# Optimization experiments

Measured on AMD Instinct MI355X. Metric: run time of the kernel, lower is better.

## Reference

```python
import jax, jax.numpy as jnp
import numpy as np

DIM = 1024
NUM_HEADS = 16
HEAD_DIM = DIM // NUM_HEADS


def setup_inputs() -> dict:
    key = jax.random.key(0)
    k1, k2, k3, k4, k5 = jax.random.split(key, 5)
    B, N, C = 4, 4096, DIM
    s = 1.0 / np.sqrt(C)
    return {
        "x": jax.random.normal(k1, (B, N, C), dtype=jnp.float32),
        "W_qkv": jax.random.uniform(k2, (C, 3 * C), dtype=jnp.float32, minval=-s, maxval=s),
        "b_qkv": jax.random.uniform(k3, (3 * C,), dtype=jnp.float32, minval=-s, maxval=s),
        "W_proj": jax.random.uniform(k4, (C, C), dtype=jnp.float32, minval=-s, maxval=s),
        "b_proj": jax.random.uniform(k5, (C,), dtype=jnp.float32, minval=-s, maxval=s),
    }


def reference(x, W_qkv, b_qkv, W_proj, b_proj):
    B, N, C = x.shape
    H, D = NUM_HEADS, HEAD_DIM
    qkv = x @ W_qkv + b_qkv                      # [B,N,3C]
    qkv = qkv.reshape(B, N, 3, H, D).transpose(2, 0, 3, 1, 4)  # [3,B,H,N,D]
    q, k, v = qkv[0], qkv[1], qkv[2]
    q = jax.nn.softmax(q, axis=-1)               # softmax over head_dim
    k = jax.nn.softmax(k, axis=-2)               # softmax over sequence N
    context = jnp.einsum('bhnd,bhne->bhde', k, v)  # [B,H,D,D]
    out = jnp.einsum('bhnd,bhde->bhne', q, context)  # [B,H,N,D]
    out = out.transpose(0, 2, 1, 3).reshape(B, N, C)
    return out @ W_proj + b_proj
```

## Files before the change

### kernel.cpp

```cpp
#include <hip/hip_runtime.h>

#define BBATCH 4
#define SEQ 4096
#define CC 1024
#define HH 16
#define DD 64
#define TOKENS 16384
#define QKV3 3072

typedef __attribute__((ext_vector_type(8))) short short8;
typedef __attribute__((ext_vector_type(4))) float floatx4;

__device__ __forceinline__ unsigned short f2bf(float x) {
    unsigned int u = __float_as_uint(x);
    u += 0x7fff + ((u >> 16) & 1);
    return (unsigned short)(u >> 16);
}
__device__ __forceinline__ float bf2f(unsigned short h) {
    return __uint_as_float((unsigned int)h << 16);
}

__device__ __forceinline__ void gload_lds16(const void* g, void* l) {
    __builtin_amdgcn_global_load_lds(
        (const __attribute__((address_space(1))) unsigned int*)g,
        (__attribute__((address_space(3))) unsigned int*)l, 16, 0, 0);
}

__global__ __launch_bounds__(256) void cvt_bf16_kernel(
    const float* __restrict__ X, unsigned short* __restrict__ Y, long n4)
{
    long i = (long)blockIdx.x * 256 + threadIdx.x;
    if (i >= n4) return;
    float4 v = *reinterpret_cast<const float4*>(&X[i * 4]);
    ushort4 h;
    h.x = f2bf(v.x); h.y = f2bf(v.y); h.z = f2bf(v.z); h.w = f2bf(v.w);
    *reinterpret_cast<ushort4*>(&Y[i * 4]) = h;
}

__global__ __launch_bounds__(256) void transpose_bf16_kernel(
    const float* __restrict__ W, int K, int N, unsigned short* __restrict__ T)
{
    __shared__ unsigned short Lh[32][36];
    const int k0 = blockIdx.y * 32, n0 = blockIdx.x * 32;
    const int t = threadIdx.x;
    const int r = t >> 3, c4 = (t & 7) * 4;

    float4 w = *reinterpret_cast<const float4*>(&W[(size_t)(k0 + r) * N + n0 + c4]);
    Lh[r][c4 + 0] = f2bf(w.x);
    Lh[r][c4 + 1] = f2bf(w.y);
    Lh[r][c4 + 2] = f2bf(w.z);
    Lh[r][c4 + 3] = f2bf(w.w);
    __syncthreads();

    const int rn = t >> 3, ck = (t & 7) * 4;
    ushort4 h4;
    h4.x = Lh[ck + 0][rn]; h4.y = Lh[ck + 1][rn];
    h4.z = Lh[ck + 2][rn]; h4.w = Lh[ck + 3][rn];
    *reinterpret_cast<ushort4*>(&T[(size_t)(n0 + rn) * K + k0 + ck]) = h4;
}

__global__ __launch_bounds__(512) void gemm_qkv_kernel(
    const unsigned short* __restrict__ A, int lda,
    const unsigned short* __restrict__ Bt, int ldb,
    const float* __restrict__ bias,
    unsigned short* __restrict__ Qo, unsigned short* __restrict__ Ko,
    unsigned short* __restrict__ Vo)
{
    __shared__ unsigned short smem[65536];

    const int t = threadIdx.x;
    const int wave = t >> 6, lane = t & 63;

    const int gx = gridDim.x;
    const int nwg = gx * gridDim.y;
    const int id0 = blockIdx.y * gx + blockIdx.x;
    const int cpx = nwg >> 3;
    const int swzid = (id0 & 7) * cpx + (id0 >> 3);
    const int bx = swzid % gx, by = swzid / gx;

    const int row0 = by * 256, col0 = bx * 256;
    const int wave_m = wave >> 2, wave_n = wave & 3;

    const unsigned short* Bp = Bt;

    const int fr  = lane & 15;
    const int fqb = (lane >> 4) << 4;
    const int sm  = (fr & 7) << 4;
    const int ck0 = ((0  + fqb) ^ sm) >> 1;
    const int ck1 = ((64 + fqb) ^ sm) >> 1;
    const int aRow = (wave_m * 128 + fr) * 64;
    const int bRow = (wave_n * 64 + fr) * 64;

    int srow[2], scol[2];
#pragma unroll
    for (int e = 0; e < 2; e++) {
        const int P  = (wave << 10) + (lane << 4) + (e << 13);
        const int r  = P >> 7;
        const int pc = P & 127;
        srow[e] = r;
        scol[e] = (pc ^ ((r & 7) << 4)) >> 1;
    }

    auto STAGE_PART = [&](int kt, int buf, int part) {
        const int isB = part >> 1, half = part & 1;
        const unsigned short* p = isB ? Bp : A;
        const int r0 = isB ? col0 : row0;
        const int ld = isB ? ldb : lda;
        const int ldsOff = buf * 32768 + isB * 16384 + half * 8192 + wave * 512;
#pragma unroll
        for (int e = 0; e < 2; e++)
            gload_lds16(&p[(size_t)(r0 + half * 128 + srow[e]) * ld
                           + ((kt & 15) << 6) + scol[e]],
                        &smem[ldsOff + e * 4096]);
    };

    floatx4 acc[8][4];
#pragma unroll
    for (int i = 0; i < 8; i++)
#pragma unroll
        for (int j = 0; j < 4; j++) acc[i][j] = (floatx4)0.0f;

    short8 a[4][2], bl[2][2], bh[2][2];

#define RDA(BUF, IH)                                                          \
    _Pragma("unroll") for (int ii = 0; ii < 4; ii++) {                        \
        a[ii][0] = *reinterpret_cast<const short8*>(                          \
            &smem[(BUF) * 32768 + aRow + ((IH) * 64 + ii * 16) * 64 + ck0]);  \
        a[ii][1] = *reinterpret_cast<const short8*>(                          \
            &smem[(BUF) * 32768 + aRow + ((IH) * 64 + ii * 16) * 64 + ck1]);  \
    }
#define RDB(BUF, JH, DST)                                                     \
    _Pragma("unroll") for (int jj = 0; jj < 2; jj++) {                        \
        DST[jj][0] = *reinterpret_cast<const short8*>(                        \
            &smem[(BUF) * 32768 + 16384 + bRow + ((JH) * 32 + jj * 16) * 64 + ck0]); \
        DST[jj][1] = *reinterpret_cast<const short8*>(                        \
            &smem[(BUF) * 32768 + 16384 + bRow + ((JH) * 32 + jj * 16) * 64 + ck1]); \
    }
#define MFMA_Q(IH, JH, BB)                                                    \
    __builtin_amdgcn_s_setprio(1);                                            \
    _Pragma("unroll") for (int ii = 0; ii < 4; ii++)                          \
    _Pragma("unroll") for (int jj = 0; jj < 2; jj++) {                        \
        acc[(IH)*4+ii][(JH)*2+jj] = __builtin_amdgcn_mfma_f32_16x16x32_bf16(  \
            a[ii][0], BB[jj][0], acc[(IH)*4+ii][(JH)*2+jj], 0, 0, 0);         \
        acc[(IH)*4+ii][(JH)*2+jj] = __builtin_amdgcn_mfma_f32_16x16x32_bf16(  \
            a[ii][1], BB[jj][1], acc[(IH)*4+ii][(JH)*2+jj], 0, 0, 0);         \
    }                                                                         \
    __builtin_amdgcn_s_setprio(0);
#define BARRIER __builtin_amdgcn_s_barrier()
#define WAIT_LGKM asm volatile("s_waitcnt lgkmcnt(0)" ::: "memory")
#define WAIT_VM2  asm volatile("s_waitcnt vmcnt(2)" ::: "memory")

#define KTILE(CUR, OTH, TN, TX)                                               \
    {                                                                         \
        RDA(CUR, 0); RDB(CUR, 0, bl);                                         \
        STAGE_PART(TN, OTH, 1);                                               \
        BARRIER; WAIT_LGKM; MFMA_Q(0, 0, bl); BARRIER;                        \
        RDB(CUR, 1, bh);                                                      \
        STAGE_PART(TN, OTH, 2);                                               \
        BARRIER; WAIT_LGKM; MFMA_Q(0, 1, bh); BARRIER;                        \
        RDA(CUR, 1);                                                          \
        STAGE_PART(TN, OTH, 3);                                               \
        BARRIER; WAIT_LGKM; MFMA_Q(1, 1, bh); BARRIER;                        \
        STAGE_PART(TX, CUR, 0);                                               \
        WAIT_VM2;                                                             \
        BARRIER;                                                              \
        MFMA_Q(1, 0, bl);                                                     \
        BARRIER;                                                              \
    }

    STAGE_PART(0, 0, 0); STAGE_PART(0, 0, 1);
    STAGE_PART(0, 0, 2); STAGE_PART(0, 0, 3);
    STAGE_PART(1, 1, 0);
    WAIT_VM2;
    BARRIER;

#pragma unroll 1
    for (int it = 0; it < 8; it++) {
        const int t1 = 2 * it + 1, t2 = 2 * it + 2, t3 = 2 * it + 3;
        KTILE(0, 1, t1, t2);
        KTILE(1, 0, t2, t3);
    }

#undef KTILE
#undef WAIT_VM2
#undef WAIT_LGKM
#undef BARRIER
#undef MFMA_Q
#undef RDB
#undef RDA

    const int cn = lane & 15, cq = (lane >> 4) * 4;

    __syncthreads();

#pragma unroll
    for (int j = 0; j < 4; j++) {
        const int colL = wave_n * 64 + j * 16 + cn;
        const float bv = bias[col0 + colL];
#pragma unroll
        for (int i = 0; i < 8; i++)
#pragma unroll
            for (int r = 0; r < 4; r++) {
                const int lr = wave_m * 128 + i * 16 + cq + r;
                smem[lr * 256 + (colL ^ ((lr & 7) << 3))] = f2bf(acc[i][j][r] + bv);
            }
    }
    __syncthreads();

    {
        unsigned short* outp = (bx < 4) ? Qo : ((bx < 8) ? Ko : Vo);
        const bool isQ = (bx < 4);
        const int R = t >> 1, half = t & 1;
        const size_t obase = (size_t)(row0 + R) * CC + (col0 & 1023) + half * 128;
        unsigned short* orow = &outp[obase];

#pragma unroll
        for (int g = 0; g < 2; g++) {
            short8 bufv[8];
            const int cbase = half * 16 + g * 8;
#pragma unroll
            for (int k = 0; k < 8; k++)
                bufv[k] = *reinterpret_cast<const short8*>(
                    &smem[R * 256 + (((cbase + k) ^ (R & 7)) << 3)]);
            if (isQ) {
                float v[64];
                float mx = -3.0e38f;
#pragma unroll
                for (int k = 0; k < 8; k++)
#pragma unroll
                    for (int e = 0; e < 8; e++) {
                        const float f = bf2f((unsigned short)bufv[k][e]);
                        v[k * 8 + e] = f;
                        mx = fmaxf(mx, f);
                    }
                float s = 0.0f;
#pragma unroll
                for (int q = 0; q < 64; q++) {
                    const float ev = __expf(v[q] - mx);
                    v[q] = ev;
                    s += ev;
                }
                const float inv = 1.0f / s;
#pragma unroll
                for (int k = 0; k < 8; k++)
#pragma unroll
                    for (int e = 0; e < 8; e++)
                        bufv[k][e] = (short)f2bf(v[k * 8 + e] * inv);
            }
#pragma unroll
            for (int k = 0; k < 8; k++)
                *reinterpret_cast<short8*>(&orow[g * 64 + k * 8]) = bufv[k];
        }
    }
}

__global__ __launch_bounds__(512) void gemm_out_kernel(
    const unsigned short* __restrict__ A, int lda,
    const unsigned short* __restrict__ Bt, int ldb,
    const float* __restrict__ bias,
    float* __restrict__ Cf, int ldc)
{
    __shared__ unsigned short smem[49152];

    const int t = threadIdx.x;
    const int wave = t >> 6, lane = t & 63;

    const int gx = gridDim.x;
    const int nwg = gx * gridDim.y;
    const int id0 = blockIdx.y * gx + blockIdx.x;
    const int cpx = nwg >> 3;
    const int swzid = (id0 & 7) * cpx + (id0 >> 3);
    const int bx = swzid % gx, by = swzid / gx;

    const int row0 = by * 256, col0 = bx * 128;
    const int wave_m = wave >> 2, wave_n = wave & 3;

    const unsigned short* Bp = Bt + (((size_t)(row0 >> 12)) << 20);

    const int fr  = lane & 15;
    const int fqb = (lane >> 4) << 4;
    const int sm  = (fr & 7) << 4;
    const int ck0 = ((0  + fqb) ^ sm) >> 1;
    const int ck1 = ((64 + fqb) ^ sm) >> 1;
    const int aRow = (wave_m * 128 + fr) * 64;
    const int bRow = (wave_n * 32 + fr) * 64;

    int srow[2], scol[2];
#pragma unroll
    for (int e = 0; e < 2; e++) {
        const int P  = (wave << 10) + (lane << 4) + (e << 13);
        const int r  = P >> 7;
        const int pc = P & 127;
        srow[e] = r;
        scol[e] = (pc ^ ((r & 7) << 4)) >> 1;
    }

    auto STAGE_PART = [&](int kt, int buf, int part) {
        const int isB = (part == 2);
        const unsigned short* p = isB ? Bp : A;
        const int r0 = isB ? col0 : (row0 + (part & 1) * 128);
        const int ld = isB ? ldb : lda;
        const int ldsOff = buf * 24576 + (isB ? 16384 : (part & 1) * 8192) + wave * 512;
#pragma unroll
        for (int e = 0; e < 2; e++)
            gload_lds16(&p[(size_t)(r0 + srow[e]) * ld
                           + ((kt & 15) << 6) + scol[e]],
                        &smem[ldsOff + e * 4096]);
    };

    floatx4 acc[8][2];
#pragma unroll
    for (int i = 0; i < 8; i++)
#pragma unroll
        for (int j = 0; j < 2; j++) acc[i][j] = (floatx4)0.0f;

    short8 a[4][2], bb[2][2];

#define RDA(BUF, IH)                                                          \
    _Pragma("unroll") for (int ii = 0; ii < 4; ii++) {                        \
        a[ii][0] = *reinterpret_cast<const short8*>(                          \
            &smem[(BUF) * 24576 + aRow + ((IH) * 64 + ii * 16) * 64 + ck0]);  \
        a[ii][1] = *reinterpret_cast<const short8*>(                          \
            &smem[(BUF) * 24576 + aRow + ((IH) * 64 + ii * 16) * 64 + ck1]);  \
    }
#define RDB(BUF)                                                              \
    _Pragma("unroll") for (int jj = 0; jj < 2; jj++) {                        \
        bb[jj][0] = *reinterpret_cast<const short8*>(                         \
            &smem[(BUF) * 24576 + 16384 + bRow + (jj * 16) * 64 + ck0]);      \
        bb[jj][1] = *reinterpret_cast<const short8*>(                         \
            &smem[(BUF) * 24576 + 16384 + bRow + (jj * 16) * 64 + ck1]);      \
    }
#define MFMA_8(IH, J)                                                         \
    __builtin_amdgcn_s_setprio(1);                                            \
    _Pragma("unroll") for (int ii = 0; ii < 4; ii++) {                        \
        acc[(IH)*4+ii][(J)] = __builtin_amdgcn_mfma_f32_16x16x32_bf16(        \
            a[ii][0], bb[(J)][0], acc[(IH)*4+ii][(J)], 0, 0, 0);              \
        acc[(IH)*4+ii][(J)] = __builtin_amdgcn_mfma_f32_16x16x32_bf16(        \
            a[ii][1], bb[(J)][1], acc[(IH)*4+ii][(J)], 0, 0, 0);              \
    }                                                                         \
    __builtin_amdgcn_s_setprio(0);
#define BARRIER __builtin_amdgcn_s_barrier()
#define WAIT_LGKM asm volatile("s_waitcnt lgkmcnt(0)" ::: "memory")
#define WAIT_VM2  asm volatile("s_waitcnt vmcnt(2)" ::: "memory")

#define KTILE(CUR, OTH, TN, TX)                                               \
    {                                                                         \
        RDA(CUR, 0); RDB(CUR);                                                \
        STAGE_PART(TN, OTH, 1);                                               \
        BARRIER; WAIT_LGKM; MFMA_8(0, 0); BARRIER;                            \
        STAGE_PART(TN, OTH, 2);                                               \
        BARRIER; MFMA_8(0, 1); BARRIER;                                       \
        RDA(CUR, 1);                                                          \
        BARRIER; WAIT_LGKM; MFMA_8(1, 1); BARRIER;                            \
        STAGE_PART(TX, CUR, 0);                                               \
        WAIT_VM2;                                                             \
        BARRIER;                                                              \
        MFMA_8(1, 0);                                                         \
        BARRIER;                                                              \
    }

    STAGE_PART(0, 0, 0); STAGE_PART(0, 0, 1); STAGE_PART(0, 0, 2);
    STAGE_PART(1, 1, 0);
    WAIT_VM2;
    BARRIER;

#pragma unroll 1
    for (int it = 0; it < 8; it++) {
        const int t1 = 2 * it + 1, t2 = 2 * it + 2, t3 = 2 * it + 3;
        KTILE(0, 1, t1, t2);
        KTILE(1, 0, t2, t3);
    }

#undef KTILE
#undef WAIT_VM2
#undef WAIT_LGKM
#undef BARRIER
#undef MFMA_8
#undef RDB
#undef RDA

    const int cn = lane & 15, cq = (lane >> 4) * 4;
#pragma unroll
    for (int j = 0; j < 2; j++) {
        const int col = col0 + wave_n * 32 + j * 16 + cn;
        const float bv = bias[col];
#pragma unroll
        for (int i = 0; i < 8; i++)
#pragma unroll
            for (int r = 0; r < 4; r++) {
                const int row = row0 + wave_m * 128 + i * 16 + cq + r;
                Cf[(size_t)row * ldc + col] = acc[i][j][r] + bv;
            }
    }
}

__global__ __launch_bounds__(256) void kv_ctx_kernel(
    const unsigned short* __restrict__ Km, const unsigned short* __restrict__ Vm,
    float* __restrict__ ctx_p, float* __restrict__ csum_p)
{
    const int bh = blockIdx.x, ch = blockIdx.y;
    const int b = bh >> 4, h = bh & 15;
    const int t = threadIdx.x;

    __shared__ float Ks[32][68];
    __shared__ float Vs[32][68];
    __shared__ float cred[4][64];

    const int d0 = (t >> 4) * 4, e0 = (t & 15) * 4;
    float acc[4][4];
#pragma unroll
    for (int i = 0; i < 4; i++)
#pragma unroll
        for (int j = 0; j < 4; j++) acc[i][j] = 0.0f;
    float csacc = 0.0f;
    const int dc = t & 63, rq = (t >> 6) * 8;

    const size_t base = (size_t)(b * SEQ + ch * 256) * CC + (size_t)h * 64;
    const int lr = t >> 3, lc = (t & 7) * 8;

    for (int n0 = 0; n0 < 256; n0 += 32) {
        __syncthreads();
        {
            short8 k8 = *reinterpret_cast<const short8*>(&Km[base + (size_t)(n0 + lr) * CC + lc]);
            short8 v8 = *reinterpret_cast<const short8*>(&Vm[base + (size_t)(n0 + lr) * CC + lc]);
            float4 ka, kb, va, vb;
            ka.x = __expf(bf2f((unsigned short)k8[0]));
            ka.y = __expf(bf2f((unsigned short)k8[1]));
            ka.z = __expf(bf2f((unsigned short)k8[2]));
            ka.w = __expf(bf2f((unsigned short)k8[3]));
            kb.x = __expf(bf2f((unsigned short)k8[4]));
            kb.y = __expf(bf2f((unsigned short)k8[5]));
            kb.z = __expf(bf2f((unsigned short)k8[6]));
            kb.w = __expf(bf2f((unsigned short)k8[7]));
            va.x = bf2f((unsigned short)v8[0]); va.y = bf2f((unsigned short)v8[1]);
            va.z = bf2f((unsigned short)v8[2]); va.w = bf2f((unsigned short)v8[3]);
            vb.x = bf2f((unsigned short)v8[4]); vb.y = bf2f((unsigned short)v8[5]);
            vb.z = bf2f((unsigned short)v8[6]); vb.w = bf2f((unsigned short)v8[7]);
            *reinterpret_cast<float4*>(&Ks[lr][lc])     = ka;
            *reinterpret_cast<float4*>(&Ks[lr][lc + 4]) = kb;
            *reinterpret_cast<float4*>(&Vs[lr][lc])     = va;
            *reinterpret_cast<float4*>(&Vs[lr][lc + 4]) = vb;
        }
        __syncthreads();

#pragma unroll
        for (int r = 0; r < 8; r++) csacc += Ks[rq + r][dc];

#pragma unroll 8
        for (int n = 0; n < 32; n++) {
            float4 a = *reinterpret_cast<const float4*>(&Ks[n][d0]);
            float4 v4 = *reinterpret_cast<const float4*>(&Vs[n][e0]);
            float a4[4] = {a.x, a.y, a.z, a.w};
            float b4[4] = {v4.x, v4.y, v4.z, v4.w};
#pragma unroll
            for (int i = 0; i < 4; i++)
#pragma unroll
                for (int j = 0; j < 4; j++)
                    acc[i][j] += a4[i] * b4[j];
        }
    }

    __syncthreads();
    cred[t >> 6][dc] = csacc;
    __syncthreads();

    const size_t pslot = (size_t)ch * 64 + bh;
    if (t < 64)
        csum_p[pslot * 64 + t] =
            cred[0][t] + cred[1][t] + cred[2][t] + cred[3][t];

    float* cp = &ctx_p[pslot * 4096];
#pragma unroll
    for (int i = 0; i < 4; i++) {
        float4 v4;
        v4.x = acc[i][0]; v4.y = acc[i][1]; v4.z = acc[i][2]; v4.w = acc[i][3];
        *reinterpret_cast<float4*>(&cp[(d0 + i) * 64 + e0]) = v4;
    }
}

__global__ __launch_bounds__(256) void reduce_ctx_kernel(
    const float* __restrict__ ctx_p, const float* __restrict__ csum_p,
    float* __restrict__ ctx, float* __restrict__ csum)
{
    const int bh = blockIdx.x, q = blockIdx.y;
    const int t = threadIdx.x;
#pragma unroll
    for (int e = 0; e < 4; e++) {
        const int idx = (q * 4 + e) * 256 + t;
        float s = 0.0f;
#pragma unroll
        for (int p = 0; p < 16; p++)
            s += ctx_p[((size_t)p * 64 + bh) * 4096 + idx];
        ctx[(size_t)bh * 4096 + idx] = s;
    }
    if (q == 0 && t < 64) {
        float s = 0.0f;
#pragma unroll
        for (int p = 0; p < 16; p++)
            s += csum_p[((size_t)p * 64 + bh) * 64 + t];
        csum[(size_t)bh * 64 + t] = s;
    }
}

__global__ __launch_bounds__(256) void weff_kernel(
    const float* __restrict__ ctx, const float* __restrict__ csum,
    const float* __restrict__ Wp, unsigned short* __restrict__ WeffT)
{
    const int bh = blockIdx.x, nc = blockIdx.y;
    const int b = bh >> 4, h = bh & 15;
    const int t = threadIdx.x;

    __shared__ float ctxsT[64 * 68];
    __shared__ float WpS[64 * 128];
    __shared__ float cinvs[64];

#pragma unroll
    for (int l = 0; l < 16; l++) {
        const int idx = t + l * 256;
        ctxsT[(idx & 63) * 68 + (idx >> 6)] = ctx[(size_t)bh * 4096 + idx];
    }
#pragma unroll
    for (int l = 0; l < 32; l++) {
        const int idx = t + l * 256;
        WpS[idx] = Wp[(size_t)(h * 64 + (idx >> 7)) * CC + nc * 128 + (idx & 127)];
    }
    if (t < 64) cinvs[t] = 1.0f / csum[(size_t)bh * 64 + t];
    __syncthreads();

    const int d0 = (t >> 5) * 8;
    const int n0 = (t & 31) * 4;

    float acc[8][4];
#pragma unroll
    for (int i = 0; i < 8; i++)
#pragma unroll
        for (int j = 0; j < 4; j++) acc[i][j] = 0.0f;

#pragma unroll 4
    for (int e = 0; e < 64; e++) {
        float4 c0 = *reinterpret_cast<const float4*>(&ctxsT[e * 68 + d0]);
        float4 c1 = *reinterpret_cast<const float4*>(&ctxsT[e * 68 + d0 + 4]);
        float4 w4 = *reinterpret_cast<const float4*>(&WpS[e * 128 + n0]);
        const float cc[8] = {c0.x, c0.y, c0.z, c0.w, c1.x, c1.y, c1.z, c1.w};
        const float ww[4] = {w4.x, w4.y, w4.z, w4.w};
#pragma unroll
        for (int i = 0; i < 8; i++)
#pragma unroll
            for (int j = 0; j < 4; j++)
                acc[i][j] += cc[i] * ww[j];
    }

    const size_t obase = ((size_t)b << 20) + (size_t)(nc * 128 + n0) * CC + h * 64 + d0;
#pragma unroll
    for (int j = 0; j < 4; j++) {
        short8 o;
#pragma unroll
        for (int i = 0; i < 8; i++)
            o[i] = (short)f2bf(acc[i][j] * cinvs[d0 + i]);
        *reinterpret_cast<short8*>(&WeffT[obase + (size_t)j * CC]) = o;
    }
}

extern "C" void kernel_launch(void* const* d_in, const int* in_sizes, int n_in,
                              void* d_out, int out_size, void* d_ws, size_t ws_size,
                              hipStream_t stream)
{
    const float* x      = (const float*)d_in[0];
    const float* W_qkv  = (const float*)d_in[1];
    const float* b_qkv  = (const float*)d_in[2];
    const float* W_proj = (const float*)d_in[3];
    const float* b_proj = (const float*)d_in[4];
    float* out = (float*)d_out;

    unsigned short* Qm  = (unsigned short*)d_ws;
    unsigned short* Km  = Qm + (size_t)TOKENS * CC;
    unsigned short* Vm  = Km + (size_t)TOKENS * CC;
    unsigned short* xb  = Vm + (size_t)TOKENS * CC;
    unsigned short* wqT = xb + (size_t)TOKENS * CC;
    unsigned short* WeffT = wqT + (size_t)QKV3 * CC;
    float* ctx    = (float*)(WeffT + (size_t)BBATCH * CC * CC);
    float* csum   = ctx + (size_t)64 * 4096;
    float* ctx_p  = (float*)xb;
    float* csum_p = ctx_p + (size_t)16 * 64 * 4096;

    cvt_bf16_kernel<<<(TOKENS * CC / 4 + 255) / 256, 256, 0, stream>>>(
        x, xb, (long)TOKENS * CC / 4);
    transpose_bf16_kernel<<<dim3(QKV3 / 32, CC / 32), 256, 0, stream>>>(
        W_qkv, CC, QKV3, wqT);

    gemm_qkv_kernel<<<dim3(QKV3 / 256, TOKENS / 256), 512, 0, stream>>>(
        xb, CC, wqT, CC, b_qkv, Qm, Km, Vm);

    kv_ctx_kernel<<<dim3(BBATCH * HH, 16), 256, 0, stream>>>(Km, Vm, ctx_p, csum_p);

    reduce_ctx_kernel<<<dim3(BBATCH * HH, 4), 256, 0, stream>>>(
        ctx_p, csum_p, ctx, csum);

    weff_kernel<<<dim3(BBATCH * HH, 8), 256, 0, stream>>>(ctx, csum, W_proj, WeffT);

    gemm_out_kernel<<<dim3(CC / 128, TOKENS / 256), 512, 0, stream>>>(
        Qm, CC, WeffT, CC, b_proj, out, CC);
}
```

Baseline: 364.6 us.

## Widen output GEMM tile to 256x256 and halve kv_ctx split count

```diff
diff --git a/kernel.cpp b/kernel.cpp
--- a/kernel.cpp
+++ b/kernel.cpp
@@ -260,7 +260,7 @@
     const float* __restrict__ bias,
     float* __restrict__ Cf, int ldc)
 {
-    __shared__ unsigned short smem[49152];
+    __shared__ unsigned short smem[65536];
 
     const int t = threadIdx.x;
     const int wave = t >> 6, lane = t & 63;
@@ -272,7 +272,7 @@
     const int swzid = (id0 & 7) * cpx + (id0 >> 3);
     const int bx = swzid % gx, by = swzid / gx;
 
-    const int row0 = by * 256, col0 = bx * 128;
+    const int row0 = by * 256, col0 = bx * 256;
     const int wave_m = wave >> 2, wave_n = wave & 3;
 
     const unsigned short* Bp = Bt + (((size_t)(row0 >> 12)) << 20);
@@ -283,7 +283,7 @@
     const int ck0 = ((0  + fqb) ^ sm) >> 1;
     const int ck1 = ((64 + fqb) ^ sm) >> 1;
     const int aRow = (wave_m * 128 + fr) * 64;
-    const int bRow = (wave_n * 32 + fr) * 64;
+    const int bRow = (wave_n * 64 + fr) * 64;
 
     int srow[2], scol[2];
 #pragma unroll
@@ -296,47 +296,48 @@
     }
 
     auto STAGE_PART = [&](int kt, int buf, int part) {
-        const int isB = (part == 2);
+        const int isB = part >> 1, half = part & 1;
         const unsigned short* p = isB ? Bp : A;
-        const int r0 = isB ? col0 : (row0 + (part & 1) * 128);
+        const int r0 = isB ? col0 : row0;
         const int ld = isB ? ldb : lda;
-        const int ldsOff = buf * 24576 + (isB ? 16384 : (part & 1) * 8192) + wave * 512;
+        const int ldsOff = buf * 32768 + isB * 16384 + half * 8192 + wave * 512;
 #pragma unroll
         for (int e = 0; e < 2; e++)
-            gload_lds16(&p[(size_t)(r0 + srow[e]) * ld
+            gload_lds16(&p[(size_t)(r0 + half * 128 + srow[e]) * ld
                            + ((kt & 15) << 6) + scol[e]],
                         &smem[ldsOff + e * 4096]);
     };
 
-    floatx4 acc[8][2];
+    floatx4 acc[8][4];
 #pragma unroll
     for (int i = 0; i < 8; i++)
 #pragma unroll
-        for (int j = 0; j < 2; j++) acc[i][j] = (floatx4)0.0f;
-
-    short8 a[4][2], bb[2][2];
+        for (int j = 0; j < 4; j++) acc[i][j] = (floatx4)0.0f;
+
+    short8 a[4][2], bl[2][2], bh[2][2];
 
 #define RDA(BUF, IH)                                                          \
     _Pragma("unroll") for (int ii = 0; ii < 4; ii++) {                        \
         a[ii][0] = *reinterpret_cast<const short8*>(                          \
-            &smem[(BUF) * 24576 + aRow + ((IH) * 64 + ii * 16) * 64 + ck0]);  \
+            &smem[(BUF) * 32768 + aRow + ((IH) * 64 + ii * 16) * 64 + ck0]);  \
         a[ii][1] = *reinterpret_cast<const short8*>(                          \
-            &smem[(BUF) * 24576 + aRow + ((IH) * 64 + ii * 16) * 64 + ck1]);  \
-    }
-#define RDB(BUF)                                                              \
+            &smem[(BUF) * 32768 + aRow + ((IH) * 64 + ii * 16) * 64 + ck1]);  \
+    }
+#define RDB(BUF, JH, DST)                                                     \
     _Pragma("unroll") for (int jj = 0; jj < 2; jj++) {                        \
-        bb[jj][0] = *reinterpret_cast<const short8*>(                         \
-            &smem[(BUF) * 24576 + 16384 + bRow + (jj * 16) * 64 + ck0]);      \
-        bb[jj][1] = *reinterpret_cast<const short8*>(                         \
-            &smem[(BUF) * 24576 + 16384 + bRow + (jj * 16) * 64 + ck1]);      \
-    }
-#define MFMA_8(IH, J)                                                         \
+        DST[jj][0] = *reinterpret_cast<const short8*>(                        \
+            &smem[(BUF) * 32768 + 16384 + bRow + ((JH) * 32 + jj * 16) * 64 + ck0]); \
+        DST[jj][1] = *reinterpret_cast<const short8*>(                        \
+            &smem[(BUF) * 32768 + 16384 + bRow + ((JH) * 32 + jj * 16) * 64 + ck1]); \
+    }
+#define MFMA_Q(IH, JH, BB)                                                    \
     __builtin_amdgcn_s_setprio(1);                                            \
-    _Pragma("unroll") for (int ii = 0; ii < 4; ii++) {                        \
-        acc[(IH)*4+ii][(J)] = __builtin_amdgcn_mfma_f32_16x16x32_bf16(        \
-            a[ii][0], bb[(J)][0], acc[(IH)*4+ii][(J)], 0, 0, 0);              \
-        acc[(IH)*4+ii][(J)] = __builtin_amdgcn_mfma_f32_16x16x32_bf16(        \
-            a[ii][1], bb[(J)][1], acc[(IH)*4+ii][(J)], 0, 0, 0);              \
+    _Pragma("unroll") for (int ii = 0; ii < 4; ii++)                          \
+    _Pragma("unroll") for (int jj = 0; jj < 2; jj++) {                        \
+        acc[(IH)*4+ii][(JH)*2+jj] = __builtin_amdgcn_mfma_f32_16x16x32_bf16(  \
+            a[ii][0], BB[jj][0], acc[(IH)*4+ii][(JH)*2+jj], 0, 0, 0);         \
+        acc[(IH)*4+ii][(JH)*2+jj] = __builtin_amdgcn_mfma_f32_16x16x32_bf16(  \
+            a[ii][1], BB[jj][1], acc[(IH)*4+ii][(JH)*2+jj], 0, 0, 0);         \
     }                                                                         \
     __builtin_amdgcn_s_setprio(0);
 #define BARRIER __builtin_amdgcn_s_barrier()
@@ -345,21 +346,24 @@
 
 #define KTILE(CUR, OTH, TN, TX)                                               \
     {                                                                         \
-        RDA(CUR, 0); RDB(CUR);                                                \
+        RDA(CUR, 0); RDB(CUR, 0, bl);                                         \
         STAGE_PART(TN, OTH, 1);                                               \
-        BARRIER; WAIT_LGKM; MFMA_8(0, 0); BARRIER;                            \
+        BARRIER; WAIT_LGKM; MFMA_Q(0, 0, bl); BARRIER;                        \
+        RDB(CUR, 1, bh);                                                      \
         STAGE_PART(TN, OTH, 2);                                               \
-        BARRIER; MFMA_8(0, 1); BARRIER;                                       \
+        BARRIER; WAIT_LGKM; MFMA_Q(0, 1, bh); BARRIER;                        \
         RDA(CUR, 1);                                                          \
-        BARRIER; WAIT_LGKM; MFMA_8(1, 1); BARRIER;                            \
+        STAGE_PART(TN, OTH, 3);                                               \
+        BARRIER; WAIT_LGKM; MFMA_Q(1, 1, bh); BARRIER;                        \
         STAGE_PART(TX, CUR, 0);                                               \
         WAIT_VM2;                                                             \
         BARRIER;                                                              \
-        MFMA_8(1, 0);                                                         \
+        MFMA_Q(1, 0, bl);                                                     \
         BARRIER;                                                              \
     }
 
-    STAGE_PART(0, 0, 0); STAGE_PART(0, 0, 1); STAGE_PART(0, 0, 2);
+    STAGE_PART(0, 0, 0); STAGE_PART(0, 0, 1);
+    STAGE_PART(0, 0, 2); STAGE_PART(0, 0, 3);
     STAGE_PART(1, 1, 0);
     WAIT_VM2;
     BARRIER;
@@ -375,14 +379,14 @@
 #undef WAIT_VM2
 #undef WAIT_LGKM
 #undef BARRIER
-#undef MFMA_8
+#undef MFMA_Q
 #undef RDB
 #undef RDA
 
     const int cn = lane & 15, cq = (lane >> 4) * 4;
 #pragma unroll
-    for (int j = 0; j < 2; j++) {
-        const int col = col0 + wave_n * 32 + j * 16 + cn;
+    for (int j = 0; j < 4; j++) {
+        const int col = col0 + wave_n * 64 + j * 16 + cn;
         const float bv = bias[col];
 #pragma unroll
         for (int i = 0; i < 8; i++)
@@ -415,10 +419,10 @@
     float csacc = 0.0f;
     const int dc = t & 63, rq = (t >> 6) * 8;
 
-    const size_t base = (size_t)(b * SEQ + ch * 256) * CC + (size_t)h * 64;
+    const size_t base = (size_t)(b * SEQ + ch * 512) * CC + (size_t)h * 64;
     const int lr = t >> 3, lc = (t & 7) * 8;
 
-    for (int n0 = 0; n0 < 256; n0 += 32) {
+    for (int n0 = 0; n0 < 512; n0 += 32) {
         __syncthreads();
         {
             short8 k8 = *reinterpret_cast<const short8*>(&Km[base + (size_t)(n0 + lr) * CC + lc]);
@@ -489,14 +493,14 @@
         const int idx = (q * 4 + e) * 256 + t;
         float s = 0.0f;
 #pragma unroll
-        for (int p = 0; p < 16; p++)
+        for (int p = 0; p < 8; p++)
             s += ctx_p[((size_t)p * 64 + bh) * 4096 + idx];
         ctx[(size_t)bh * 4096 + idx] = s;
     }
     if (q == 0 && t < 64) {
         float s = 0.0f;
 #pragma unroll
-        for (int p = 0; p < 16; p++)
+        for (int p = 0; p < 8; p++)
             s += csum_p[((size_t)p * 64 + bh) * 64 + t];
         csum[(size_t)bh * 64 + t] = s;
     }
@@ -581,7 +585,7 @@
     float* ctx    = (float*)(WeffT + (size_t)BBATCH * CC * CC);
     float* csum   = ctx + (size_t)64 * 4096;
     float* ctx_p  = (float*)xb;
-    float* csum_p = ctx_p + (size_t)16 * 64 * 4096;
+    float* csum_p = ctx_p + (size_t)8 * 64 * 4096;
 
     cvt_bf16_kernel<<<(TOKENS * CC / 4 + 255) / 256, 256, 0, stream>>>(
         x, xb, (long)TOKENS * CC / 4);
@@ -591,13 +595,13 @@
     gemm_qkv_kernel<<<dim3(QKV3 / 256, TOKENS / 256), 512, 0, stream>>>(
         xb, CC, wqT, CC, b_qkv, Qm, Km, Vm);
 
-    kv_ctx_kernel<<<dim3(BBATCH * HH, 16), 256, 0, stream>>>(Km, Vm, ctx_p, csum_p);
+    kv_ctx_kernel<<<dim3(BBATCH * HH, 8), 256, 0, stream>>>(Km, Vm, ctx_p, csum_p);
 
     reduce_ctx_kernel<<<dim3(BBATCH * HH, 4), 256, 0, stream>>>(
         ctx_p, csum_p, ctx, csum);
 
     weff_kernel<<<dim3(BBATCH * HH, 8), 256, 0, stream>>>(ctx, csum, W_proj, WeffT);
 
-    gemm_out_kernel<<<dim3(CC / 128, TOKENS / 256), 512, 0, stream>>>(
+    gemm_out_kernel<<<dim3(CC / 256, TOKENS / 256), 512, 0, stream>>>(
         Qm, CC, WeffT, CC, b_proj, out, CC);
 }
```

New measurement: 359.5 us. About the same (-1.4%).
